# Kernel tuning notes

Hardware: AMD Instinct MI355X
Metric: run time of the kernel (lower is better)

## Reference

```python
import jax, jax.numpy as jnp
import numpy as np

N = 100000
E = 3200000
D_IN = 256
D_OUT = 128
ALPHA = 0.2  # tf.nn.leaky_relu default slope


def setup_inputs() -> dict:
    key = jax.random.key(0)
    ks = jax.random.split(key, 8)
    feat = jax.random.normal(ks[0], (N, D_IN), dtype=jnp.float32)
    row = jax.random.randint(ks[1], (E,), 0, N, dtype=jnp.int32)
    col = jax.random.randint(ks[2], (E,), 0, N, dtype=jnp.int32)
    # Dense(out_dim, use_bias=False)
    W = jax.random.normal(ks[3], (D_IN, D_OUT), dtype=jnp.float32) / np.sqrt(D_IN)
    # attn_l / attn_r: Dense(1) with bias
    al_w = jax.random.normal(ks[4], (D_OUT, 1), dtype=jnp.float32) / np.sqrt(D_OUT)
    al_b = jnp.zeros((1,), dtype=jnp.float32)
    ar_w = jax.random.normal(ks[5], (D_OUT, 1), dtype=jnp.float32) / np.sqrt(D_OUT)
    ar_b = jnp.zeros((1,), dtype=jnp.float32)
    bias = jnp.zeros((D_OUT,), dtype=jnp.float32)
    return {"feat": feat, "row": row, "col": col, "W": W,
            "al_w": al_w, "al_b": al_b, "ar_w": ar_w, "ar_b": ar_b, "bias": bias}


def reference(feat, row, col, W, al_w, al_b, ar_w, ar_b, bias):
    # seq_fts = W(feat)  [N, D_OUT]
    seq_fts = feat @ W
    # per-node attention scalars  [N]
    f1 = (seq_fts @ al_w + al_b)[:, 0]
    f2 = (seq_fts @ ar_w + ar_b)[:, 0]
    # per-edge logits (gather) + leaky_relu  [E]
    logits = jax.nn.leaky_relu(f1[row] + f2[col], negative_slope=ALPHA)
    # sparse (segment) softmax over each destination row
    m = jax.ops.segment_max(logits, row, num_segments=N)   # [N], -inf for empty rows (unused)
    e = jnp.exp(logits - m[row])                            # [E]
    s = jax.ops.segment_sum(e, row, num_segments=N)         # [N]
    coefs = e / s[row]                                      # [E]
    # spmm: vals[i] = sum_{e: row[e]=i} coefs[e] * seq_fts[col[e]]
    vals = jax.ops.segment_sum(coefs[:, None] * seq_fts[col], row, num_segments=N)
    return vals + bias  # act is None
```

## Files before the change

### kernel.cpp

```cpp
#include <hip/hip_runtime.h>
#include <math.h>

#define N_NODES 100000
#define N_EDGES 3200000
#define D_IN    256
#define D_OUT   128
#define ALPHA   0.2f

#define NB_HIST 125
#define CHUNK   (N_EDGES / NB_HIST)
#define HWORDS  (N_NODES / 4)
#define NGRP    5
#define GLEN    (NB_HIST / NGRP)

typedef short bf8_t  __attribute__((ext_vector_type(8)));
typedef float f4_t   __attribute__((ext_vector_type(4)));

__device__ __forceinline__ unsigned int f2bf(float x) {
    unsigned int u = __float_as_uint(x);
    return (u + 0x7fffu + ((u >> 16) & 1u)) >> 16;
}
__device__ __forceinline__ unsigned int packbf(float lo, float hi) {
    return f2bf(lo) | (f2bf(hi) << 16);
}
__device__ __forceinline__ float bflo(unsigned int v) { return __uint_as_float(v << 16); }
__device__ __forceinline__ float bfhi(unsigned int v) { return __uint_as_float(v & 0xffff0000u); }

__global__ void wt_kernel(const float* __restrict__ W, short* __restrict__ WTs) {
    int o = blockIdx.x * 256 + threadIdx.x;
    int j    = o & 7;
    int lane = (o >> 3) & 63;
    int nt   = (o >> 9) & 7;
    int kc   = o >> 12;
    int n = nt * 16 + (lane & 15);
    int k = kc * 32 + (lane >> 4) * 8 + j;
    WTs[o] = (short)f2bf(W[k * 128 + n]);
}

__global__ __launch_bounds__(256) void gemm_kernel(const float* __restrict__ feat,
                                                   const short* __restrict__ WTs,
                                                   const float* __restrict__ al_w,
                                                   const float* __restrict__ al_b,
                                                   const float* __restrict__ ar_w,
                                                   const float* __restrict__ ar_b,
                                                   unsigned int* __restrict__ seqb,
                                                   float* __restrict__ f1,
                                                   float* __restrict__ f2) {
    __shared__ char ldsA[64 * 528];
    const int tid = threadIdx.x;
    const int tb  = blockIdx.x * 64;

#pragma unroll
    for (int i = 0; i < 16; i++) {
        int idx = i * 256 + tid;
        int r   = idx >> 6;
        int c4  = idx & 63;
        int gr  = tb + r; if (gr >= N_NODES) gr = N_NODES - 1;
        float4 v = ((const float4*)feat)[(size_t)gr * 64 + c4];
        *(uint2*)(ldsA + r * 528 + c4 * 8) =
            make_uint2(packbf(v.x, v.y), packbf(v.z, v.w));
    }
    __syncthreads();

    const int w    = tid >> 6;
    const int lane = tid & 63;
    const int m    = lane & 15;
    const int q    = lane >> 4;

    const char*  aptr = ldsA + (w * 16 + m) * 528 + q * 16;
    const short* bb   = WTs + (size_t)lane * 8;

    f4_t acc[8];
#pragma unroll
    for (int nt = 0; nt < 8; nt++) acc[nt] = (f4_t)(0.f);

#pragma unroll
    for (int kc = 0; kc < 8; kc++) {
        bf8_t a = *(const bf8_t*)(aptr + kc * 64);
#pragma unroll
        for (int nt = 0; nt < 8; nt++) {
            bf8_t b = *(const bf8_t*)(bb + (kc * 8 + nt) * 512);
            acc[nt] = __builtin_amdgcn_mfma_f32_16x16x32_bf16(a, b, acc[nt], 0, 0, 0);
        }
    }

    const int node_base = tb + w * 16 + q * 4;
#pragma unroll
    for (int nt = 0; nt < 8; nt++) {
#pragma unroll
        for (int j = 0; j < 4; j++) {
            float own   = acc[nt][j];
            float other = __shfl_xor(own, 1);
            int node = node_base + j;
            if (!(lane & 1) && node < N_NODES)
                seqb[(size_t)node * 64 + nt * 8 + (m >> 1)] = packbf(own, other);
        }
    }

    float p1[4] = {0.f, 0.f, 0.f, 0.f}, p2[4] = {0.f, 0.f, 0.f, 0.f};
#pragma unroll
    for (int nt = 0; nt < 8; nt++) {
        float av = al_w[nt * 16 + m];
        float rv = ar_w[nt * 16 + m];
#pragma unroll
        for (int j = 0; j < 4; j++) {
            p1[j] += acc[nt][j] * av;
            p2[j] += acc[nt][j] * rv;
        }
    }
#pragma unroll
    for (int j = 0; j < 4; j++) {
#pragma unroll
        for (int mk = 1; mk < 16; mk <<= 1) {
            p1[j] += __shfl_xor(p1[j], mk);
            p2[j] += __shfl_xor(p2[j], mk);
        }
    }
    if (m == 0) {
        float alb = al_b[0], arb = ar_b[0];
#pragma unroll
        for (int j = 0; j < 4; j++) {
            int node = node_base + j;
            if (node < N_NODES) {
                f1[node] = p1[j] + alb;
                f2[node] = p2[j] + arb;
            }
        }
    }
}

__global__ __launch_bounds__(1024) void hist_kernel(const int* __restrict__ row,
                                                    unsigned char* __restrict__ localrank,
                                                    unsigned int* __restrict__ histpk) {
    __shared__ unsigned int h[HWORDS];
    const int tid = threadIdx.x;
    for (int i = tid; i < HWORDS; i += 1024) h[i] = 0u;
    __syncthreads();

    const int base = blockIdx.x * CHUNK;
#pragma unroll
    for (int it = 0; it < CHUNK / 1024; it++) {
        int e = base + it * 1024 + tid;
        int r = row[e];
        unsigned int sh  = (unsigned int)(r & 3) * 8u;
        unsigned int old = atomicAdd(&h[r >> 2], 1u << sh);
        localrank[e] = (unsigned char)((old >> sh) & 0xffu);
    }
    __syncthreads();

    unsigned int* dst = histpk + (size_t)blockIdx.x * HWORDS;
    for (int i = tid; i < HWORDS; i += 1024) dst[i] = h[i];
}

__global__ __launch_bounds__(256) void scanbA_kernel(const unsigned int* __restrict__ histpk,
                                                     unsigned int* __restrict__ blockpre,
                                                     unsigned int* __restrict__ gsum) {
    int id = blockIdx.x * 256 + threadIdx.x;
    if (id >= NGRP * HWORDS) return;
    int g = id / HWORDS;
    int w = id - g * HWORDS;
    const unsigned int* hp = histpk   + (size_t)(g * GLEN) * HWORDS + w;
    unsigned int*       bp = blockpre + (size_t)(g * GLEN) * HWORDS + w;
    unsigned int run = 0u;
#pragma unroll 5
    for (int i = 0; i < GLEN; i++) {
        unsigned int hv = hp[(size_t)i * HWORDS];
        bp[(size_t)i * HWORDS] = run;
        run += hv;
    }
    gsum[(size_t)g * HWORDS + w] = run;
}

__global__ __launch_bounds__(256) void degscan_kernel(unsigned int* __restrict__ gsum,
                                                      uint4* __restrict__ cnt4,
                                                      unsigned int* __restrict__ offs,
                                                      unsigned int* __restrict__ bsums) {
    __shared__ unsigned int s[256];
    const int t = threadIdx.x;
    const int w = blockIdx.x * 256 + t;
    unsigned int run = 0u, T = 0u;
    unsigned int d0 = 0, d1 = 0, d2 = 0;
    if (w < HWORDS) {
#pragma unroll
        for (int g = 0; g < NGRP; g++) {
            unsigned int v = gsum[(size_t)g * HWORDS + w];
            gsum[(size_t)g * HWORDS + w] = run;
            run += v;
        }
        cnt4[w] = make_uint4(run & 0xffu, (run >> 8) & 0xffu,
                             (run >> 16) & 0xffu, run >> 24);
        d0 = run & 0xffu; d1 = (run >> 8) & 0xffu; d2 = (run >> 16) & 0xffu;
        T = d0 + d1 + d2 + (run >> 24);
    }
    s[t] = T; __syncthreads();
    for (int d = 1; d < 256; d <<= 1) {
        unsigned int x = (t >= d) ? s[t - d] : 0u;
        __syncthreads();
        s[t] += x;
        __syncthreads();
    }
    if (w < HWORDS) {
        unsigned int excl = s[t] - T;
        offs[w * 4 + 0] = excl;
        offs[w * 4 + 1] = excl + d0;
        offs[w * 4 + 2] = excl + d0 + d1;
        offs[w * 4 + 3] = excl + d0 + d1 + d2;
    }
    if (t == 255) bsums[blockIdx.x] = s[255];
}

__global__ void scan2(const unsigned int* __restrict__ bsums,
                      unsigned int* __restrict__ bexcl, int nb) {
    __shared__ unsigned int s[512];
    int t = threadIdx.x;
    unsigned int v = (t < nb) ? bsums[t] : 0u;
    s[t] = v; __syncthreads();
    for (int d = 1; d < 512; d <<= 1) {
        unsigned int x = (t >= d) ? s[t - d] : 0u;
        __syncthreads();
        s[t] += x;
        __syncthreads();
    }
    if (t < nb) bexcl[t] = s[t] - v;
}

__global__ __launch_bounds__(256) void scan3g_kernel(unsigned int* __restrict__ offs,
                                                     const unsigned int* __restrict__ bexcl,
                                                     const unsigned int* __restrict__ gsum,
                                                     unsigned int* __restrict__ offs_g) {
    int i = blockIdx.x * 256 + threadIdx.x;
    if (i >= N_NODES) return;
    unsigned int o = offs[i] + bexcl[i >> 10];
    offs[i] = o;
    unsigned int sh = (unsigned int)(i & 3) * 8u;
#pragma unroll
    for (int g = 0; g < NGRP; g++) {
        unsigned int gb = (gsum[(size_t)g * HWORDS + (i >> 2)] >> sh) & 0xffu;
        offs_g[(size_t)g * N_NODES + i] = o + gb;
    }
}

__global__ __launch_bounds__(512) void scatter_kernel(const int* __restrict__ row,
                                                      const int* __restrict__ col,
                                                      const unsigned char* __restrict__ localrank,
                                                      const unsigned int* __restrict__ blockpre,
                                                      const unsigned int* __restrict__ offs_g,
                                                      int* __restrict__ sorted_c) {
    __shared__ unsigned int wpre[HWORDS];
    const int b    = blockIdx.x >> 1;
    const int half = blockIdx.x & 1;
    const int tid  = threadIdx.x;

    const unsigned int* src = blockpre + (size_t)b * HWORDS;
    for (int i = tid; i < HWORDS; i += 512) wpre[i] = src[i];
    __syncthreads();

    const unsigned int* og = offs_g + (size_t)(b / GLEN) * N_NODES;
    const int base = b * CHUNK + half * (CHUNK / 2);
#pragma unroll 5
    for (int it = 0; it < (CHUNK / 2) / 512; it++) {
        int e = base + it * 512 + tid;
        int r = row[e];
        unsigned int bp = (wpre[r >> 2] >> ((unsigned int)(r & 3) * 8u)) & 0xffu;
        unsigned int p  = og[r] + bp + (unsigned int)localrank[e];
        sorted_c[p] = col[e];
    }
}

__device__ __forceinline__ void row_body(int wid_base,
                                         const uint4* __restrict__ seqb4,
                                         const int* __restrict__ sorted_c,
                                         const unsigned int* __restrict__ offs,
                                         const unsigned int* __restrict__ cnt,
                                         const float* __restrict__ f1,
                                         const float* __restrict__ f2,
                                         const float* __restrict__ bias,
                                         float* __restrict__ out) {
    int wid  = wid_base + ((blockIdx.x * 256 + threadIdx.x) >> 6);
    int lane = threadIdx.x & 63;
    int g    = lane >> 4;
    int j4   = lane & 15;
    unsigned int start = offs[wid];
    unsigned int deg   = cnt[wid];
    const int* sc = sorted_c + start;
    float f1r = f1[wid];

    float a0 = 0.f, a1 = 0.f, a2 = 0.f, a3 = 0.f;
    float a4 = 0.f, a5 = 0.f, a6 = 0.f, a7 = 0.f, ss = 0.f;

    unsigned int k = 0;
    for (; k + 16 <= deg; k += 16) {
        int c0 = sc[k + g];
        int c1 = sc[k + 4 + g];
        int c2 = sc[k + 8 + g];
        int c3 = sc[k + 12 + g];
        uint4 v0 = seqb4[(unsigned)c0 * 16u + j4];
        uint4 v1 = seqb4[(unsigned)c1 * 16u + j4];
        uint4 v2 = seqb4[(unsigned)c2 * 16u + j4];
        uint4 v3 = seqb4[(unsigned)c3 * 16u + j4];
        float t0 = f1r + f2[c0], t1 = f1r + f2[c1];
        float t2 = f1r + f2[c2], t3 = f1r + f2[c3];
        float w0 = __expf(fmaxf(t0, ALPHA * t0));
        float w1 = __expf(fmaxf(t1, ALPHA * t1));
        float w2 = __expf(fmaxf(t2, ALPHA * t2));
        float w3 = __expf(fmaxf(t3, ALPHA * t3));
        ss += (w0 + w1) + (w2 + w3);
        a0 += w0 * bflo(v0.x); a1 += w0 * bfhi(v0.x);
        a2 += w0 * bflo(v0.y); a3 += w0 * bfhi(v0.y);
        a4 += w0 * bflo(v0.z); a5 += w0 * bfhi(v0.z);
        a6 += w0 * bflo(v0.w); a7 += w0 * bfhi(v0.w);
        a0 += w1 * bflo(v1.x); a1 += w1 * bfhi(v1.x);
        a2 += w1 * bflo(v1.y); a3 += w1 * bfhi(v1.y);
        a4 += w1 * bflo(v1.z); a5 += w1 * bfhi(v1.z);
        a6 += w1 * bflo(v1.w); a7 += w1 * bfhi(v1.w);
        a0 += w2 * bflo(v2.x); a1 += w2 * bfhi(v2.x);
        a2 += w2 * bflo(v2.y); a3 += w2 * bfhi(v2.y);
        a4 += w2 * bflo(v2.z); a5 += w2 * bfhi(v2.z);
        a6 += w2 * bflo(v2.w); a7 += w2 * bfhi(v2.w);
        a0 += w3 * bflo(v3.x); a1 += w3 * bfhi(v3.x);
        a2 += w3 * bflo(v3.y); a3 += w3 * bfhi(v3.y);
        a4 += w3 * bflo(v3.z); a5 += w3 * bfhi(v3.z);
        a6 += w3 * bflo(v3.w); a7 += w3 * bfhi(v3.w);
    }
    for (; k + 8 <= deg; k += 8) {
        int ca = sc[k + g];
        int cb = sc[k + 4 + g];
        uint4 va = seqb4[(unsigned)ca * 16u + j4];
        uint4 vb = seqb4[(unsigned)cb * 16u + j4];
        float ta = f1r + f2[ca];
        float tb = f1r + f2[cb];
        float wa = __expf(fmaxf(ta, ALPHA * ta));
        float wb = __expf(fmaxf(tb, ALPHA * tb));
        ss += wa + wb;
        a0 += wa * bflo(va.x); a1 += wa * bfhi(va.x);
        a2 += wa * bflo(va.y); a3 += wa * bfhi(va.y);
        a4 += wa * bflo(va.z); a5 += wa * bfhi(va.z);
        a6 += wa * bflo(va.w); a7 += wa * bfhi(va.w);
        a0 += wb * bflo(vb.x); a1 += wb * bfhi(vb.x);
        a2 += wb * bflo(vb.y); a3 += wb * bfhi(vb.y);
        a4 += wb * bflo(vb.z); a5 += wb * bfhi(vb.z);
        a6 += wb * bflo(vb.w); a7 += wb * bfhi(vb.w);
    }
    for (; k < deg; k += 4) {
        unsigned int ke = k + g;
        int c = sc[ke < deg ? ke : deg - 1];
        uint4 v = seqb4[(unsigned)c * 16u + j4];
        float t = f1r + f2[c];
        float w = __expf(fmaxf(t, ALPHA * t));
        if (ke >= deg) w = 0.f;
        ss += w;
        a0 += w * bflo(v.x); a1 += w * bfhi(v.x);
        a2 += w * bflo(v.y); a3 += w * bfhi(v.y);
        a4 += w * bflo(v.z); a5 += w * bfhi(v.z);
        a6 += w * bflo(v.w); a7 += w * bfhi(v.w);
    }

    a0 += __shfl_xor(a0, 16); a0 += __shfl_xor(a0, 32);
    a1 += __shfl_xor(a1, 16); a1 += __shfl_xor(a1, 32);
    a2 += __shfl_xor(a2, 16); a2 += __shfl_xor(a2, 32);
    a3 += __shfl_xor(a3, 16); a3 += __shfl_xor(a3, 32);
    a4 += __shfl_xor(a4, 16); a4 += __shfl_xor(a4, 32);
    a5 += __shfl_xor(a5, 16); a5 += __shfl_xor(a5, 32);
    a6 += __shfl_xor(a6, 16); a6 += __shfl_xor(a6, 32);
    a7 += __shfl_xor(a7, 16); a7 += __shfl_xor(a7, 32);
    ss += __shfl_xor(ss, 16); ss += __shfl_xor(ss, 32);

    if (g == 0) {
        float inv = (deg > 0) ? 1.f / ss : 0.f;
        float4 b0 = ((const float4*)bias)[j4 * 2];
        float4 b1 = ((const float4*)bias)[j4 * 2 + 1];
        float4* orow = (float4*)(out + (size_t)wid * D_OUT);
        orow[j4 * 2]     = make_float4(a0 * inv + b0.x, a1 * inv + b0.y,
                                       a2 * inv + b0.z, a3 * inv + b0.w);
        orow[j4 * 2 + 1] = make_float4(a4 * inv + b1.x, a5 * inv + b1.y,
                                       a6 * inv + b1.z, a7 * inv + b1.w);
    }
}

__global__ __launch_bounds__(256) void rowA_kernel(const uint4* __restrict__ seqb4,
                                                   const int* __restrict__ sorted_c,
                                                   const unsigned int* __restrict__ offs,
                                                   const unsigned int* __restrict__ cnt,
                                                   const float* __restrict__ f1,
                                                   const float* __restrict__ f2,
                                                   const float* __restrict__ bias,
                                                   float* __restrict__ out) {
    row_body(0, seqb4, sorted_c, offs, cnt, f1, f2, bias, out);
}
__global__ __launch_bounds__(256) void rowB_kernel(const uint4* __restrict__ seqb4,
                                                   const int* __restrict__ sorted_c,
                                                   const unsigned int* __restrict__ offs,
                                                   const unsigned int* __restrict__ cnt,
                                                   const float* __restrict__ f1,
                                                   const float* __restrict__ f2,
                                                   const float* __restrict__ bias,
                                                   float* __restrict__ out) {
    row_body(N_NODES / 2, seqb4, sorted_c, offs, cnt, f1, f2, bias, out);
}

extern "C" void kernel_launch(void* const* d_in, const int* in_sizes, int n_in,
                              void* d_out, int out_size, void* d_ws, size_t ws_size,
                              hipStream_t stream) {
    const float* feat = (const float*)d_in[0];
    const int*   row  = (const int*)d_in[1];
    const int*   col  = (const int*)d_in[2];
    const float* W    = (const float*)d_in[3];
    const float* al_w = (const float*)d_in[4];
    const float* al_b = (const float*)d_in[5];
    const float* ar_w = (const float*)d_in[6];
    const float* ar_b = (const float*)d_in[7];
    const float* bias = (const float*)d_in[8];
    float* out = (float*)d_out;

    char* ws = (char*)d_ws;
    size_t off = 0;
    auto carve = [&](size_t bytes) -> void* {
        off = (off + 255) & ~(size_t)255;
        void* p = ws + off;
        off += bytes;
        return p;
    };
    unsigned int* seqb     = (unsigned int*)carve((size_t)N_NODES * 64 * 4);
    float*        f1       = (float*)       carve((size_t)N_NODES * 4);
    float*        f2       = (float*)       carve((size_t)N_NODES * 4);
    unsigned int* cnt      = (unsigned int*)carve((size_t)N_NODES * 4);
    unsigned int* offs     = (unsigned int*)carve((size_t)N_NODES * 4);
    unsigned int* bsums    = (unsigned int*)carve(1024 * 4);
    unsigned int* bexcl    = (unsigned int*)carve(1024 * 4);
    short*        WTs      = (short*)       carve((size_t)D_IN * D_OUT * 2);
    unsigned char* localrank = (unsigned char*)carve((size_t)N_EDGES);
    unsigned int* blockpre = (unsigned int*)carve((size_t)NB_HIST * HWORDS * 4);
    unsigned int* gsum     = (unsigned int*)carve((size_t)NGRP * HWORDS * 4);
    unsigned int* offs_g   = (unsigned int*)carve((size_t)NGRP * N_NODES * 4);
    int*          sorted_c = (int*)         carve((size_t)N_EDGES * 4);
    unsigned int* histpk   = (unsigned int*)sorted_c;
    (void)ws_size; (void)in_sizes; (void)n_in; (void)out_size;

    const int nb_nodes = (N_NODES + 255) / 256;
    const int nb_gemm  = (N_NODES + 63) / 64;
    const int nb_gw    = (NGRP * HWORDS + 255) / 256;
    const int nb_deg   = (HWORDS + 255) / 256;
    const int nb_rowh  = (N_NODES / 2) / 4;

    wt_kernel<<<(D_IN * D_OUT) / 256, 256, 0, stream>>>(W, WTs);
    gemm_kernel<<<nb_gemm, 256, 0, stream>>>(feat, WTs, al_w, al_b, ar_w, ar_b, seqb, f1, f2);
    hist_kernel<<<NB_HIST, 1024, 0, stream>>>(row, localrank, histpk);
    scanbA_kernel<<<nb_gw, 256, 0, stream>>>(histpk, blockpre, gsum);
    degscan_kernel<<<nb_deg, 256, 0, stream>>>(gsum, (uint4*)cnt, offs, bsums);
    scan2<<<1, 512, 0, stream>>>(bsums, bexcl, nb_deg);
    scan3g_kernel<<<nb_nodes, 256, 0, stream>>>(offs, bexcl, gsum, offs_g);
    scatter_kernel<<<NB_HIST * 2, 512, 0, stream>>>(row, col, localrank,
                                                    blockpre, offs_g, sorted_c);
    rowA_kernel<<<nb_rowh, 256, 0, stream>>>((const uint4*)seqb, sorted_c, offs, cnt, f1, f2, bias, out);
    rowB_kernel<<<nb_rowh, 256, 0, stream>>>((const uint4*)seqb, sorted_c, offs, cnt, f1, f2, bias, out);
}
```

Before: 446.7 us.

## Split edge scatter into position precompute and destination-windowed multi-pass scatter

The single scatter kernel is replaced by two steps. A prep kernel computes each edge's destination slot into a buffer, reading the per-chunk prefix table from global memory instead of staging it in LDS. A scatter8 kernel then sweeps the positions and columns once per eight destination windows, writing only the edges whose slot falls in its window, so random writes stay within a smaller address range for better cache locality. In exchange, positions and columns are reread eight times and one extra kernel launch is added; workspace regions are re-aliased so the prefix table shares memory with the sorted output.

```diff
diff --git a/kernel.cpp b/kernel.cpp
--- a/kernel.cpp
+++ b/kernel.cpp
@@ -12,6 +12,9 @@
 #define HWORDS  (N_NODES / 4)
 #define NGRP    5
 #define GLEN    (NB_HIST / NGRP)
+#define NSEG    8
+#define SEGW    (N_EDGES / NSEG)
+#define SLICE   12800
 
 typedef short bf8_t  __attribute__((ext_vector_type(8)));
 typedef float f4_t   __attribute__((ext_vector_type(4)));
@@ -240,30 +243,33 @@
     }
 }
 
-__global__ __launch_bounds__(512) void scatter_kernel(const int* __restrict__ row,
-                                                      const int* __restrict__ col,
-                                                      const unsigned char* __restrict__ localrank,
-                                                      const unsigned int* __restrict__ blockpre,
-                                                      const unsigned int* __restrict__ offs_g,
-                                                      int* __restrict__ sorted_c) {
-    __shared__ unsigned int wpre[HWORDS];
-    const int b    = blockIdx.x >> 1;
-    const int half = blockIdx.x & 1;
-    const int tid  = threadIdx.x;
-
-    const unsigned int* src = blockpre + (size_t)b * HWORDS;
-    for (int i = tid; i < HWORDS; i += 512) wpre[i] = src[i];
-    __syncthreads();
-
-    const unsigned int* og = offs_g + (size_t)(b / GLEN) * N_NODES;
-    const int base = b * CHUNK + half * (CHUNK / 2);
+__global__ __launch_bounds__(256) void prep_kernel(const int* __restrict__ row,
+                                                   const unsigned char* __restrict__ localrank,
+                                                   const unsigned int* __restrict__ blockpre,
+                                                   const unsigned int* __restrict__ offs_g,
+                                                   unsigned int* __restrict__ p) {
+    int e = blockIdx.x * 256 + threadIdx.x;
+    int b = (blockIdx.x * 256) / CHUNK;
+    int r = row[e];
+    unsigned int bp = (blockpre[(size_t)b * HWORDS + (r >> 2)]
+                       >> ((unsigned int)(r & 3) * 8u)) & 0xffu;
+    p[e] = offs_g[(size_t)(b / GLEN) * N_NODES + r] + bp + (unsigned int)localrank[e];
+}
+
+__global__ __launch_bounds__(256) void scatter8_kernel(const unsigned int* __restrict__ p,
+                                                       const int* __restrict__ col,
+                                                       int* __restrict__ sorted_c) {
+    const int seg   = blockIdx.x & 7;
+    const int slice = blockIdx.x >> 3;
+    const unsigned int lo = (unsigned int)seg * SEGW;
+    const int base2 = slice * (SLICE / 2);
 #pragma unroll 5
-    for (int it = 0; it < (CHUNK / 2) / 512; it++) {
-        int e = base + it * 512 + tid;
-        int r = row[e];
-        unsigned int bp = (wpre[r >> 2] >> ((unsigned int)(r & 3) * 8u)) & 0xffu;
-        unsigned int p  = og[r] + bp + (unsigned int)localrank[e];
-        sorted_c[p] = col[e];
+    for (int it = 0; it < SLICE / 512; it++) {
+        int i2 = base2 + it * 256 + threadIdx.x;
+        uint2 pp = ((const uint2*)p)[i2];
+        int2  cc = ((const int2*)col)[i2];
+        if (pp.x - lo < (unsigned int)SEGW) sorted_c[pp.x] = cc.x;
+        if (pp.y - lo < (unsigned int)SEGW) sorted_c[pp.y] = cc.y;
     }
 }
 
@@ -429,17 +435,22 @@
     unsigned int* bexcl    = (unsigned int*)carve(1024 * 4);
     short*        WTs      = (short*)       carve((size_t)D_IN * D_OUT * 2);
     unsigned char* localrank = (unsigned char*)carve((size_t)N_EDGES);
-    unsigned int* blockpre = (unsigned int*)carve((size_t)NB_HIST * HWORDS * 4);
     unsigned int* gsum     = (unsigned int*)carve((size_t)NGRP * HWORDS * 4);
     unsigned int* offs_g   = (unsigned int*)carve((size_t)NGRP * N_NODES * 4);
-    int*          sorted_c = (int*)         carve((size_t)N_EDGES * 4);
-    unsigned int* histpk   = (unsigned int*)sorted_c;
+    unsigned int* regionA  = (unsigned int*)carve((size_t)N_EDGES * 4);
+    unsigned int* histpk   = regionA;
+    unsigned int* p        = regionA;
+    unsigned int* regionB  = (unsigned int*)carve((size_t)N_EDGES * 4);
+    unsigned int* blockpre = regionB;
+    int*          sorted_c = (int*)regionB;
     (void)ws_size; (void)in_sizes; (void)n_in; (void)out_size;
 
     const int nb_nodes = (N_NODES + 255) / 256;
     const int nb_gemm  = (N_NODES + 63) / 64;
     const int nb_gw    = (NGRP * HWORDS + 255) / 256;
     const int nb_deg   = (HWORDS + 255) / 256;
+    const int nb_prep  = N_EDGES / 256;
+    const int nb_sc8   = (N_EDGES / SLICE) * NSEG;
     const int nb_rowh  = (N_NODES / 2) / 4;
 
     wt_kernel<<<(D_IN * D_OUT) / 256, 256, 0, stream>>>(W, WTs);
@@ -449,8 +460,8 @@
     degscan_kernel<<<nb_deg, 256, 0, stream>>>(gsum, (uint4*)cnt, offs, bsums);
     scan2<<<1, 512, 0, stream>>>(bsums, bexcl, nb_deg);
     scan3g_kernel<<<nb_nodes, 256, 0, stream>>>(offs, bexcl, gsum, offs_g);
-    scatter_kernel<<<NB_HIST * 2, 512, 0, stream>>>(row, col, localrank,
-                                                    blockpre, offs_g, sorted_c);
+    prep_kernel<<<nb_prep, 256, 0, stream>>>(row, localrank, blockpre, offs_g, p);
+    scatter8_kernel<<<nb_sc8, 256, 0, stream>>>(p, col, sorted_c);
     rowA_kernel<<<nb_rowh, 256, 0, stream>>>((const uint4*)seqb, sorted_c, offs, cnt, f1, f2, bias, out);
     rowB_kernel<<<nb_rowh, 256, 0, stream>>>((const uint4*)seqb, sorted_c, offs, cnt, f1, f2, bias, out);
 }
```

Result: no change. 450.2 us (+0.8%).

## Replace random scatter of sorted columns with two-pass bucketed scatter through LDS

Applied to the files above, without the earlier changes.

The single scatter kernel, which wrote col values to random positions across the whole 12.8 MB sorted array, becomes two passes. The first pass computes each edge's final position, groups the edges into 256 coarse buckets using an LDS histogram and global cursors, and writes packed (local offset, col) records. The second pass loads each bucket into a 50 KB LDS window, places the records locally, then writes the window out with coalesced stores. This aims to turn scattered global writes into mostly coalesced ones, at the cost of an extra pass over the edges, global atomics, and buffer aliasing (blockpre now shares memory with sorted_c).

```diff
diff --git a/kernel.cpp b/kernel.cpp
--- a/kernel.cpp
+++ b/kernel.cpp
@@ -12,6 +12,9 @@
 #define HWORDS  (N_NODES / 4)
 #define NGRP    5
 #define GLEN    (NB_HIST / NGRP)
+#define NBUK    256
+#define BW      (N_EDGES / NBUK)
+#define P1TILE  12800
 
 typedef short bf8_t  __attribute__((ext_vector_type(8)));
 typedef float f4_t   __attribute__((ext_vector_type(4)));
@@ -227,7 +230,10 @@
 __global__ __launch_bounds__(256) void scan3g_kernel(unsigned int* __restrict__ offs,
                                                      const unsigned int* __restrict__ bexcl,
                                                      const unsigned int* __restrict__ gsum,
-                                                     unsigned int* __restrict__ offs_g) {
+                                                     unsigned int* __restrict__ offs_g,
+                                                     unsigned int* __restrict__ cursor) {
+    if (blockIdx.x == 0 && threadIdx.x < NBUK)
+        cursor[threadIdx.x] = (unsigned int)threadIdx.x * BW;
     int i = blockIdx.x * 256 + threadIdx.x;
     if (i >= N_NODES) return;
     unsigned int o = offs[i] + bexcl[i >> 10];
@@ -240,31 +246,66 @@
     }
 }
 
-__global__ __launch_bounds__(512) void scatter_kernel(const int* __restrict__ row,
-                                                      const int* __restrict__ col,
-                                                      const unsigned char* __restrict__ localrank,
-                                                      const unsigned int* __restrict__ blockpre,
-                                                      const unsigned int* __restrict__ offs_g,
-                                                      int* __restrict__ sorted_c) {
-    __shared__ unsigned int wpre[HWORDS];
-    const int b    = blockIdx.x >> 1;
-    const int half = blockIdx.x & 1;
-    const int tid  = threadIdx.x;
-
-    const unsigned int* src = blockpre + (size_t)b * HWORDS;
-    for (int i = tid; i < HWORDS; i += 512) wpre[i] = src[i];
-    __syncthreads();
-
+__global__ __launch_bounds__(512) void bucket_kernel(const int* __restrict__ row,
+                                                     const int* __restrict__ col,
+                                                     const unsigned char* __restrict__ localrank,
+                                                     const unsigned int* __restrict__ blockpre,
+                                                     const unsigned int* __restrict__ offs_g,
+                                                     unsigned int* __restrict__ cursor,
+                                                     unsigned int* __restrict__ records) {
+    __shared__ unsigned int pst[P1TILE];
+    __shared__ unsigned int hcnt[NBUK];
+    const int tid = threadIdx.x;
+    const int blk = blockIdx.x;
+    const int b   = blk >> 1;
+    const unsigned int* bp = blockpre + (size_t)b * HWORDS;
     const unsigned int* og = offs_g + (size_t)(b / GLEN) * N_NODES;
-    const int base = b * CHUNK + half * (CHUNK / 2);
-#pragma unroll 5
-    for (int it = 0; it < (CHUNK / 2) / 512; it++) {
-        int e = base + it * 512 + tid;
-        int r = row[e];
-        unsigned int bp = (wpre[r >> 2] >> ((unsigned int)(r & 3) * 8u)) & 0xffu;
-        unsigned int p  = og[r] + bp + (unsigned int)localrank[e];
-        sorted_c[p] = col[e];
-    }
+    if (tid < NBUK) hcnt[tid] = 0u;
+    __syncthreads();
+
+    const int base = blk * P1TILE;
+#pragma unroll
+    for (int it = 0; it < P1TILE / 512; it++) {
+        int i = it * 512 + tid;
+        int r = row[base + i];
+        unsigned int pb = (bp[r >> 2] >> ((unsigned int)(r & 3) * 8u)) & 0xffu;
+        unsigned int p  = og[r] + pb + (unsigned int)localrank[base + i];
+        pst[i] = p;
+        atomicAdd(&hcnt[p / BW], 1u);
+    }
+    __syncthreads();
+    if (tid < NBUK) {
+        unsigned int c = hcnt[tid];
+        hcnt[tid] = atomicAdd(&cursor[tid], c);
+    }
+    __syncthreads();
+#pragma unroll
+    for (int it = 0; it < P1TILE / 512; it++) {
+        int i = it * 512 + tid;
+        unsigned int p   = pst[i];
+        unsigned int buk = p / BW;
+        unsigned int idx = atomicAdd(&hcnt[buk], 1u);
+        records[idx] = ((p - buk * BW) << 17) | (unsigned int)col[base + i];
+    }
+}
+
+__global__ __launch_bounds__(256) void scatter2_kernel(const unsigned int* __restrict__ records,
+                                                       int* __restrict__ sorted_c) {
+    __shared__ int win[BW];
+    const int tid = threadIdx.x;
+    const unsigned int gb = (unsigned int)blockIdx.x * BW;
+    const uint4* rec4 = (const uint4*)(records + gb);
+    for (int i = tid; i < BW / 4; i += 256) {
+        uint4 r4 = rec4[i];
+        win[r4.x >> 17] = (int)(r4.x & 0x1FFFFu);
+        win[r4.y >> 17] = (int)(r4.y & 0x1FFFFu);
+        win[r4.z >> 17] = (int)(r4.z & 0x1FFFFu);
+        win[r4.w >> 17] = (int)(r4.w & 0x1FFFFu);
+    }
+    __syncthreads();
+    int4* dst = (int4*)(sorted_c + gb);
+    const int4* src = (const int4*)win;
+    for (int i = tid; i < BW / 4; i += 256) dst[i] = src[i];
 }
 
 __device__ __forceinline__ void row_body(int wid_base,
@@ -427,19 +468,24 @@
     unsigned int* offs     = (unsigned int*)carve((size_t)N_NODES * 4);
     unsigned int* bsums    = (unsigned int*)carve(1024 * 4);
     unsigned int* bexcl    = (unsigned int*)carve(1024 * 4);
+    unsigned int* cursor   = (unsigned int*)carve(NBUK * 4);
     short*        WTs      = (short*)       carve((size_t)D_IN * D_OUT * 2);
     unsigned char* localrank = (unsigned char*)carve((size_t)N_EDGES);
-    unsigned int* blockpre = (unsigned int*)carve((size_t)NB_HIST * HWORDS * 4);
     unsigned int* gsum     = (unsigned int*)carve((size_t)NGRP * HWORDS * 4);
     unsigned int* offs_g   = (unsigned int*)carve((size_t)NGRP * N_NODES * 4);
-    int*          sorted_c = (int*)         carve((size_t)N_EDGES * 4);
-    unsigned int* histpk   = (unsigned int*)sorted_c;
+    unsigned int* regionA  = (unsigned int*)carve((size_t)N_EDGES * 4);
+    unsigned int* histpk   = regionA;
+    unsigned int* records  = regionA;
+    unsigned int* regionB  = (unsigned int*)carve((size_t)N_EDGES * 4);
+    unsigned int* blockpre = regionB;
+    int*          sorted_c = (int*)regionB;
     (void)ws_size; (void)in_sizes; (void)n_in; (void)out_size;
 
     const int nb_nodes = (N_NODES + 255) / 256;
     const int nb_gemm  = (N_NODES + 63) / 64;
     const int nb_gw    = (NGRP * HWORDS + 255) / 256;
     const int nb_deg   = (HWORDS + 255) / 256;
+    const int nb_p1    = N_EDGES / P1TILE;
     const int nb_rowh  = (N_NODES / 2) / 4;
 
     wt_kernel<<<(D_IN * D_OUT) / 256, 256, 0, stream>>>(W, WTs);
@@ -448,9 +494,10 @@
     scanbA_kernel<<<nb_gw, 256, 0, stream>>>(histpk, blockpre, gsum);
     degscan_kernel<<<nb_deg, 256, 0, stream>>>(gsum, (uint4*)cnt, offs, bsums);
     scan2<<<1, 512, 0, stream>>>(bsums, bexcl, nb_deg);
-    scan3g_kernel<<<nb_nodes, 256, 0, stream>>>(offs, bexcl, gsum, offs_g);
-    scatter_kernel<<<NB_HIST * 2, 512, 0, stream>>>(row, col, localrank,
-                                                    blockpre, offs_g, sorted_c);
+    scan3g_kernel<<<nb_nodes, 256, 0, stream>>>(offs, bexcl, gsum, offs_g, cursor);
+    bucket_kernel<<<nb_p1, 512, 0, stream>>>(row, col, localrank, blockpre, offs_g,
+                                             cursor, records);
+    scatter2_kernel<<<NBUK, 256, 0, stream>>>(records, sorted_c);
     rowA_kernel<<<nb_rowh, 256, 0, stream>>>((const uint4*)seqb, sorted_c, offs, cnt, f1, f2, bias, out);
     rowB_kernel<<<nb_rowh, 256, 0, stream>>>((const uint4*)seqb, sorted_c, offs, cnt, f1, f2, bias, out);
 }
```

Measured after the change: 424.0 us. 5.1% less time.

## Replace per-node histogram sort with two-level bucket sort into CSR

Applied to the files above, without the earlier changes.

The CSR build by row changes from per-block packed 8-bit histograms plus multi-stage scans and a scatter to a two-pass bucket sort. Edges are first binned into 782 coarse buckets of 128 rows using global atomic cursors. Each bucket is then sorted locally in LDS to produce sorted columns, offsets and counts. This drops several kernels and the large blockpre and offs_g buffers, but the order of edges within a row becomes nondeterministic. The GEMM also loads feat rows straight from global memory into registers instead of staging them through LDS.

```diff
diff --git a/kernel.cpp b/kernel.cpp
--- a/kernel.cpp
+++ b/kernel.cpp
@@ -7,11 +7,11 @@
 #define D_OUT   128
 #define ALPHA   0.2f
 
-#define NB_HIST 125
-#define CHUNK   (N_EDGES / NB_HIST)
-#define HWORDS  (N_NODES / 4)
-#define NGRP    5
-#define GLEN    (NB_HIST / NGRP)
+#define RPB     128
+#define NBUK2   782
+#define MAXBUK  6144
+#define B2TILE  12800
+#define B2PT    (B2TILE / 512)
 
 typedef short bf8_t  __attribute__((ext_vector_type(8)));
 typedef float f4_t   __attribute__((ext_vector_type(4)));
@@ -46,29 +46,27 @@
                                                    unsigned int* __restrict__ seqb,
                                                    float* __restrict__ f1,
                                                    float* __restrict__ f2) {
-    __shared__ char ldsA[64 * 528];
-    const int tid = threadIdx.x;
-    const int tb  = blockIdx.x * 64;
-
-#pragma unroll
-    for (int i = 0; i < 16; i++) {
-        int idx = i * 256 + tid;
-        int r   = idx >> 6;
-        int c4  = idx & 63;
-        int gr  = tb + r; if (gr >= N_NODES) gr = N_NODES - 1;
-        float4 v = ((const float4*)feat)[(size_t)gr * 64 + c4];
-        *(uint2*)(ldsA + r * 528 + c4 * 8) =
-            make_uint2(packbf(v.x, v.y), packbf(v.z, v.w));
-    }
-    __syncthreads();
-
+    const int tid  = threadIdx.x;
     const int w    = tid >> 6;
     const int lane = tid & 63;
     const int m    = lane & 15;
     const int q    = lane >> 4;
-
-    const char*  aptr = ldsA + (w * 16 + m) * 528 + q * 16;
-    const short* bb   = WTs + (size_t)lane * 8;
+    const int tb   = blockIdx.x * 64;
+
+    int gr = tb + w * 16 + m; if (gr >= N_NODES) gr = N_NODES - 1;
+    const float4* fp = (const float4*)(feat + (size_t)gr * 256) + q * 2;
+
+    bf8_t a[8];
+#pragma unroll
+    for (int kc = 0; kc < 8; kc++) {
+        float4 v0 = fp[kc * 8];
+        float4 v1 = fp[kc * 8 + 1];
+        uint4 u = make_uint4(packbf(v0.x, v0.y), packbf(v0.z, v0.w),
+                             packbf(v1.x, v1.y), packbf(v1.z, v1.w));
+        a[kc] = *(const bf8_t*)&u;
+    }
+
+    const short* bb = WTs + (size_t)lane * 8;
 
     f4_t acc[8];
 #pragma unroll
@@ -76,11 +74,10 @@
 
 #pragma unroll
     for (int kc = 0; kc < 8; kc++) {
-        bf8_t a = *(const bf8_t*)(aptr + kc * 64);
 #pragma unroll
         for (int nt = 0; nt < 8; nt++) {
             bf8_t b = *(const bf8_t*)(bb + (kc * 8 + nt) * 512);
-            acc[nt] = __builtin_amdgcn_mfma_f32_16x16x32_bf16(a, b, acc[nt], 0, 0, 0);
+            acc[nt] = __builtin_amdgcn_mfma_f32_16x16x32_bf16(a[kc], b, acc[nt], 0, 0, 0);
         }
     }
 
@@ -129,141 +126,117 @@
     }
 }
 
-__global__ __launch_bounds__(1024) void hist_kernel(const int* __restrict__ row,
-                                                    unsigned char* __restrict__ localrank,
-                                                    unsigned int* __restrict__ histpk) {
-    __shared__ unsigned int h[HWORDS];
+__global__ __launch_bounds__(512) void sizes_kernel(const int* __restrict__ row,
+                                                    unsigned int* __restrict__ gsize) {
+    __shared__ unsigned int h[NBUK2];
     const int tid = threadIdx.x;
-    for (int i = tid; i < HWORDS; i += 1024) h[i] = 0u;
-    __syncthreads();
-
-    const int base = blockIdx.x * CHUNK;
-#pragma unroll
-    for (int it = 0; it < CHUNK / 1024; it++) {
-        int e = base + it * 1024 + tid;
-        int r = row[e];
-        unsigned int sh  = (unsigned int)(r & 3) * 8u;
-        unsigned int old = atomicAdd(&h[r >> 2], 1u << sh);
-        localrank[e] = (unsigned char)((old >> sh) & 0xffu);
-    }
-    __syncthreads();
-
-    unsigned int* dst = histpk + (size_t)blockIdx.x * HWORDS;
-    for (int i = tid; i < HWORDS; i += 1024) dst[i] = h[i];
-}
-
-__global__ __launch_bounds__(256) void scanbA_kernel(const unsigned int* __restrict__ histpk,
-                                                     unsigned int* __restrict__ blockpre,
-                                                     unsigned int* __restrict__ gsum) {
-    int id = blockIdx.x * 256 + threadIdx.x;
-    if (id >= NGRP * HWORDS) return;
-    int g = id / HWORDS;
-    int w = id - g * HWORDS;
-    const unsigned int* hp = histpk   + (size_t)(g * GLEN) * HWORDS + w;
-    unsigned int*       bp = blockpre + (size_t)(g * GLEN) * HWORDS + w;
-    unsigned int run = 0u;
-#pragma unroll 5
-    for (int i = 0; i < GLEN; i++) {
-        unsigned int hv = hp[(size_t)i * HWORDS];
-        bp[(size_t)i * HWORDS] = run;
-        run += hv;
-    }
-    gsum[(size_t)g * HWORDS + w] = run;
-}
-
-__global__ __launch_bounds__(256) void degscan_kernel(unsigned int* __restrict__ gsum,
-                                                      uint4* __restrict__ cnt4,
-                                                      unsigned int* __restrict__ offs,
-                                                      unsigned int* __restrict__ bsums) {
-    __shared__ unsigned int s[256];
+    for (int i = tid; i < NBUK2; i += 512) h[i] = 0u;
+    __syncthreads();
+    const int base = blockIdx.x * B2TILE;
+#pragma unroll
+    for (int it = 0; it < B2PT; it++) {
+        unsigned int r = (unsigned int)row[base + it * 512 + tid];
+        atomicAdd(&h[r >> 7], 1u);
+    }
+    __syncthreads();
+    for (int i = tid; i < NBUK2; i += 512)
+        if (h[i]) atomicAdd(&gsize[i], h[i]);
+}
+
+__global__ __launch_bounds__(1024) void scanS_kernel(const unsigned int* __restrict__ gsize,
+                                                     unsigned int* __restrict__ bukbase,
+                                                     unsigned int* __restrict__ cursor) {
+    __shared__ unsigned int s[1024];
     const int t = threadIdx.x;
-    const int w = blockIdx.x * 256 + t;
-    unsigned int run = 0u, T = 0u;
-    unsigned int d0 = 0, d1 = 0, d2 = 0;
-    if (w < HWORDS) {
-#pragma unroll
-        for (int g = 0; g < NGRP; g++) {
-            unsigned int v = gsum[(size_t)g * HWORDS + w];
-            gsum[(size_t)g * HWORDS + w] = run;
-            run += v;
-        }
-        cnt4[w] = make_uint4(run & 0xffu, (run >> 8) & 0xffu,
-                             (run >> 16) & 0xffu, run >> 24);
-        d0 = run & 0xffu; d1 = (run >> 8) & 0xffu; d2 = (run >> 16) & 0xffu;
-        T = d0 + d1 + d2 + (run >> 24);
-    }
-    s[t] = T; __syncthreads();
-    for (int d = 1; d < 256; d <<= 1) {
+    unsigned int v = (t < NBUK2) ? gsize[t] : 0u;
+    s[t] = v; __syncthreads();
+    for (int d = 1; d < 1024; d <<= 1) {
         unsigned int x = (t >= d) ? s[t - d] : 0u;
         __syncthreads();
         s[t] += x;
         __syncthreads();
     }
-    if (w < HWORDS) {
-        unsigned int excl = s[t] - T;
-        offs[w * 4 + 0] = excl;
-        offs[w * 4 + 1] = excl + d0;
-        offs[w * 4 + 2] = excl + d0 + d1;
-        offs[w * 4 + 3] = excl + d0 + d1 + d2;
-    }
-    if (t == 255) bsums[blockIdx.x] = s[255];
-}
-
-__global__ void scan2(const unsigned int* __restrict__ bsums,
-                      unsigned int* __restrict__ bexcl, int nb) {
-    __shared__ unsigned int s[512];
-    int t = threadIdx.x;
-    unsigned int v = (t < nb) ? bsums[t] : 0u;
-    s[t] = v; __syncthreads();
-    for (int d = 1; d < 512; d <<= 1) {
-        unsigned int x = (t >= d) ? s[t - d] : 0u;
+    if (t < NBUK2) {
+        unsigned int excl = s[t] - v;
+        bukbase[t] = excl;
+        cursor[t * 16] = excl;
+        if (t == NBUK2 - 1) bukbase[NBUK2] = s[t];
+    }
+}
+
+__global__ __launch_bounds__(512) void bucket2_kernel(const int* __restrict__ row,
+                                                      const int* __restrict__ col,
+                                                      unsigned int* __restrict__ cursor,
+                                                      unsigned int* __restrict__ records) {
+    __shared__ unsigned int hcnt[NBUK2];
+    const int tid = threadIdx.x;
+    const int base = blockIdx.x * B2TILE;
+    for (int i = tid; i < NBUK2; i += 512) hcnt[i] = 0u;
+    __syncthreads();
+
+    unsigned int rec[B2PT], bk[B2PT];
+#pragma unroll
+    for (int it = 0; it < B2PT; it++) {
+        int e = base + it * 512 + tid;
+        unsigned int r = (unsigned int)row[e];
+        bk[it]  = r >> 7;
+        rec[it] = ((r & 127u) << 17) | (unsigned int)col[e];
+        atomicAdd(&hcnt[bk[it]], 1u);
+    }
+    __syncthreads();
+    for (int i = tid; i < NBUK2; i += 512) {
+        unsigned int c = hcnt[i];
+        if (c) hcnt[i] = atomicAdd(&cursor[i * 16], c);
+    }
+    __syncthreads();
+#pragma unroll
+    for (int it = 0; it < B2PT; it++) {
+        unsigned int idx = atomicAdd(&hcnt[bk[it]], 1u);
+        records[idx] = rec[it];
+    }
+}
+
+__global__ __launch_bounds__(256) void csr_kernel(const unsigned int* __restrict__ records,
+                                                  const unsigned int* __restrict__ bukbase,
+                                                  int* __restrict__ sorted_c,
+                                                  unsigned int* __restrict__ offs,
+                                                  unsigned int* __restrict__ cnt) {
+    __shared__ unsigned int h[RPB], sc[RPB], cur[RPB];
+    __shared__ int win[MAXBUK];
+    const int tid = threadIdx.x;
+    const int b   = blockIdx.x;
+    const unsigned int base = bukbase[b];
+    const int nrec = (int)(bukbase[b + 1] - base);
+
+    if (tid < RPB) h[tid] = 0u;
+    __syncthreads();
+    for (int i = tid; i < nrec; i += 256)
+        atomicAdd(&h[records[base + i] >> 17], 1u);
+    __syncthreads();
+    if (tid < RPB) sc[tid] = h[tid];
+    __syncthreads();
+    for (int d = 1; d < RPB; d <<= 1) {
+        unsigned int x = (tid < RPB && tid >= d) ? sc[tid - d] : 0u;
         __syncthreads();
-        s[t] += x;
+        if (tid < RPB) sc[tid] += x;
         __syncthreads();
     }
-    if (t < nb) bexcl[t] = s[t] - v;
-}
-
-__global__ __launch_bounds__(256) void scan3g_kernel(unsigned int* __restrict__ offs,
-                                                     const unsigned int* __restrict__ bexcl,
-                                                     const unsigned int* __restrict__ gsum,
-                                                     unsigned int* __restrict__ offs_g) {
-    int i = blockIdx.x * 256 + threadIdx.x;
-    if (i >= N_NODES) return;
-    unsigned int o = offs[i] + bexcl[i >> 10];
-    offs[i] = o;
-    unsigned int sh = (unsigned int)(i & 3) * 8u;
-#pragma unroll
-    for (int g = 0; g < NGRP; g++) {
-        unsigned int gb = (gsum[(size_t)g * HWORDS + (i >> 2)] >> sh) & 0xffu;
-        offs_g[(size_t)g * N_NODES + i] = o + gb;
-    }
-}
-
-__global__ __launch_bounds__(512) void scatter_kernel(const int* __restrict__ row,
-                                                      const int* __restrict__ col,
-                                                      const unsigned char* __restrict__ localrank,
-                                                      const unsigned int* __restrict__ blockpre,
-                                                      const unsigned int* __restrict__ offs_g,
-                                                      int* __restrict__ sorted_c) {
-    __shared__ unsigned int wpre[HWORDS];
-    const int b    = blockIdx.x >> 1;
-    const int half = blockIdx.x & 1;
-    const int tid  = threadIdx.x;
-
-    const unsigned int* src = blockpre + (size_t)b * HWORDS;
-    for (int i = tid; i < HWORDS; i += 512) wpre[i] = src[i];
-    __syncthreads();
-
-    const unsigned int* og = offs_g + (size_t)(b / GLEN) * N_NODES;
-    const int base = b * CHUNK + half * (CHUNK / 2);
-#pragma unroll 5
-    for (int it = 0; it < (CHUNK / 2) / 512; it++) {
-        int e = base + it * 512 + tid;
-        int r = row[e];
-        unsigned int bp = (wpre[r >> 2] >> ((unsigned int)(r & 3) * 8u)) & 0xffu;
-        unsigned int p  = og[r] + bp + (unsigned int)localrank[e];
-        sorted_c[p] = col[e];
+    if (tid < RPB) cur[tid] = sc[tid] - h[tid];
+    __syncthreads();
+    for (int i = tid; i < nrec; i += 256) {
+        unsigned int rec = records[base + i];
+        unsigned int idx = atomicAdd(&cur[rec >> 17], 1u);
+        win[idx] = (int)(rec & 0x1FFFFu);
+    }
+    __syncthreads();
+    for (int i = tid; i < nrec; i += 256)
+        sorted_c[base + i] = win[i];
+    if (tid < RPB) {
+        int r = b * RPB + tid;
+        if (r < N_NODES) {
+            offs[r] = base + (sc[tid] - h[tid]);
+            cnt[r]  = h[tid];
+        }
     }
 }
 
@@ -425,32 +398,25 @@
     float*        f2       = (float*)       carve((size_t)N_NODES * 4);
     unsigned int* cnt      = (unsigned int*)carve((size_t)N_NODES * 4);
     unsigned int* offs     = (unsigned int*)carve((size_t)N_NODES * 4);
-    unsigned int* bsums    = (unsigned int*)carve(1024 * 4);
-    unsigned int* bexcl    = (unsigned int*)carve(1024 * 4);
     short*        WTs      = (short*)       carve((size_t)D_IN * D_OUT * 2);
-    unsigned char* localrank = (unsigned char*)carve((size_t)N_EDGES);
-    unsigned int* blockpre = (unsigned int*)carve((size_t)NB_HIST * HWORDS * 4);
-    unsigned int* gsum     = (unsigned int*)carve((size_t)NGRP * HWORDS * 4);
-    unsigned int* offs_g   = (unsigned int*)carve((size_t)NGRP * N_NODES * 4);
+    unsigned int* gsize    = (unsigned int*)carve((size_t)NBUK2 * 4);
+    unsigned int* bukbase  = (unsigned int*)carve((size_t)(NBUK2 + 1) * 4);
+    unsigned int* cursor   = (unsigned int*)carve((size_t)NBUK2 * 64);
+    unsigned int* records  = (unsigned int*)carve((size_t)N_EDGES * 4);
     int*          sorted_c = (int*)         carve((size_t)N_EDGES * 4);
-    unsigned int* histpk   = (unsigned int*)sorted_c;
     (void)ws_size; (void)in_sizes; (void)n_in; (void)out_size;
 
-    const int nb_nodes = (N_NODES + 255) / 256;
-    const int nb_gemm  = (N_NODES + 63) / 64;
-    const int nb_gw    = (NGRP * HWORDS + 255) / 256;
-    const int nb_deg   = (HWORDS + 255) / 256;
-    const int nb_rowh  = (N_NODES / 2) / 4;
-
+    const int nb_gemm = (N_NODES + 63) / 64;
+    const int nb_b2   = N_EDGES / B2TILE;
+    const int nb_rowh = (N_NODES / 2) / 4;
+
+    hipMemsetAsync(gsize, 0, (size_t)NBUK2 * 4, stream);
     wt_kernel<<<(D_IN * D_OUT) / 256, 256, 0, stream>>>(W, WTs);
     gemm_kernel<<<nb_gemm, 256, 0, stream>>>(feat, WTs, al_w, al_b, ar_w, ar_b, seqb, f1, f2);
-    hist_kernel<<<NB_HIST, 1024, 0, stream>>>(row, localrank, histpk);
-    scanbA_kernel<<<nb_gw, 256, 0, stream>>>(histpk, blockpre, gsum);
-    degscan_kernel<<<nb_deg, 256, 0, stream>>>(gsum, (uint4*)cnt, offs, bsums);
-    scan2<<<1, 512, 0, stream>>>(bsums, bexcl, nb_deg);
-    scan3g_kernel<<<nb_nodes, 256, 0, stream>>>(offs, bexcl, gsum, offs_g);
-    scatter_kernel<<<NB_HIST * 2, 512, 0, stream>>>(row, col, localrank,
-                                                    blockpre, offs_g, sorted_c);
+    sizes_kernel<<<nb_b2, 512, 0, stream>>>(row, gsize);
+    scanS_kernel<<<1, 1024, 0, stream>>>(gsize, bukbase, cursor);
+    bucket2_kernel<<<nb_b2, 512, 0, stream>>>(row, col, cursor, records);
+    csr_kernel<<<NBUK2, 256, 0, stream>>>(records, bukbase, sorted_c, offs, cnt);
     rowA_kernel<<<nb_rowh, 256, 0, stream>>>((const uint4*)seqb, sorted_c, offs, cnt, f1, f2, bias, out);
     rowB_kernel<<<nb_rowh, 256, 0, stream>>>((const uint4*)seqb, sorted_c, offs, cnt, f1, f2, bias, out);
 }
```

After: 387.9 us. 1.15x faster.
